# Kernel optimization log

Hardware: AMD Instinct MI355X
Metric: run time of the kernel (lower is better)

## Reference

```python
import jax, jax.numpy as jnp
import numpy as np

NEG = -1e9


def setup_inputs() -> dict:
    key = jax.random.key(0)
    ks = jax.random.split(key, 10)
    B, C, H, W = 4, 64, 64, 64
    Cq = C // 8
    x = jax.random.normal(ks[0], (B, C, H, W), dtype=jnp.float32)
    mask = jax.random.randint(ks[1], (B, 1, H, W), 0, 2, dtype=jnp.int32)
    # 1x1 conv params (out_ch, in_ch) + bias
    Wq = jax.random.normal(ks[2], (Cq, C), dtype=jnp.float32) * (1.0 / np.sqrt(C))
    bq = jnp.zeros((Cq,), dtype=jnp.float32)
    Wk = jax.random.normal(ks[3], (Cq, C), dtype=jnp.float32) * (1.0 / np.sqrt(C))
    bk = jnp.zeros((Cq,), dtype=jnp.float32)
    Wv = jax.random.normal(ks[4], (C, C), dtype=jnp.float32) * (1.0 / np.sqrt(C))
    bv = jnp.zeros((C,), dtype=jnp.float32)
    # torch inits gamma to 0; use small random so attention path contributes
    gamma = jax.random.normal(ks[5], (1,), dtype=jnp.float32) * 0.1
    return {"x": x, "mask": mask, "Wq": Wq, "bq": bq, "Wk": Wk, "bk": bk,
            "Wv": Wv, "bv": bv, "gamma": gamma}


def reference(x, mask, Wq, bq, Wk, bk, Wv, bv, gamma):
    B, C, H, W = x.shape
    N = H * W
    xf = x.reshape(B, C, N)                      # (B,C,N)
    # 1x1 convs == per-pixel linear projections
    q = jnp.einsum('oc,bcn->bno', Wq, xf) + bq   # (B,N,Cq)
    k = jnp.einsum('oc,bcn->bon', Wk, xf) + bk[None, :, None]  # (B,Cq,N)
    v = jnp.einsum('oc,bcn->bon', Wv, xf) + bv[None, :, None]  # (B,C,N)
    m = mask.reshape(B, N).astype(bool)
    logits = jnp.einsum('bno,bom->bnm', q, k)    # (B,N,N)
    valid = m[:, :, None] & m[:, None, :]        # outer-product validity mask
    logits = jnp.where(valid, logits, NEG)
    attn = jax.nn.softmax(logits, axis=-1)       # (B,N,N)
    out = jnp.einsum('bcj,bij->bci', v, attn)    # (B,C,N)
    out = out.reshape(B, C, H, W)
    return gamma * out + x
```

## Files before the change

### kernel.cpp

```cpp
#include <hip/hip_runtime.h>

typedef unsigned int uint;
typedef unsigned short ushort;
typedef __attribute__((ext_vector_type(8))) short short8;
typedef __attribute__((ext_vector_type(4))) float f32x4;
typedef __attribute__((ext_vector_type(16))) float f32x16;
typedef __attribute__((ext_vector_type(4))) uint uint4v;

#define BATCH 4
#define CH 64
#define NPIX 4096
#define LOG2E 1.44269504f

#define WSQ 0
#define WSK (BATCH * 128 * 512)
#define WSV (2 * BATCH * 128 * 512)

__device__ __forceinline__ ushort f2bf(float f) {
    union { float f; uint u; } a; a.f = f;
    const uint u = a.u;
    return (ushort)((u + 0x7FFFu + ((u >> 16) & 1u)) >> 16);
}
__device__ __forceinline__ uint pkbf(float a, float b) {
    return (uint)f2bf(a) | ((uint)f2bf(b) << 16);
}
__device__ __forceinline__ uint pkbf_fu(float a, float b) {
    union { float f; uint u; } x, y; x.f = a; y.f = b;
    return ((y.u + 0x8000u) & 0xFFFF0000u) | ((x.u + 0x8000u) >> 16);
}

__global__ __launch_bounds__(256) void proj_kernel(
    const float* __restrict__ x, const int* __restrict__ mask,
    const float* __restrict__ Wq, const float* __restrict__ bq,
    const float* __restrict__ Wk, const float* __restrict__ bk,
    const float* __restrict__ Wv, const float* __restrict__ bv,
    ushort* __restrict__ ws)
{
    __shared__ float wsh[16 * 64];
    __shared__ float bsh[16];
    const int g = blockIdx.y;
    const int tid = threadIdx.x;
    const int nout = (g == 0) ? 16 : 8;

    if (g == 0) {
        for (int i = tid; i < 512; i += 256) { wsh[i] = Wq[i]; wsh[512 + i] = Wk[i]; }
        if (tid < 8)  bsh[tid] = bq[tid];
        else if (tid < 16) bsh[tid] = bk[tid - 8];
    } else {
        const float* W = Wv + (g - 1) * 512;
        for (int i = tid; i < 512; i += 256) wsh[i] = W[i];
        if (tid < 8) bsh[tid] = bv[(g - 1) * 8 + tid];
    }
    __syncthreads();

    const int pix = blockIdx.x * 256 + tid;
    const int b = pix >> 12;
    const int n = pix & (NPIX - 1);
    const float* xb = x + (size_t)b * CH * NPIX + n;

    float acc[16];
#pragma unroll
    for (int o = 0; o < 16; o++) acc[o] = (o < nout) ? bsh[o] : 0.f;

#pragma unroll
    for (int c4 = 0; c4 < 16; c4++) {
        float xv0 = xb[(size_t)(c4 * 4 + 0) * NPIX];
        float xv1 = xb[(size_t)(c4 * 4 + 1) * NPIX];
        float xv2 = xb[(size_t)(c4 * 4 + 2) * NPIX];
        float xv3 = xb[(size_t)(c4 * 4 + 3) * NPIX];
        if (g == 0) {
#pragma unroll
            for (int o = 0; o < 16; o++) {
                const int base = (o < 8 ? 0 : 512) + (o & 7) * 64;
                float4 w = *(const float4*)&wsh[base + c4 * 4];
                acc[o] += w.x * xv0 + w.y * xv1 + w.z * xv2 + w.w * xv3;
            }
        } else {
#pragma unroll
            for (int o = 0; o < 8; o++) {
                float4 w = *(const float4*)&wsh[o * 64 + c4 * 4];
                acc[o] += w.x * xv0 + w.y * xv1 + w.z * xv2 + w.w * xv3;
            }
        }
    }

    const int jt = n >> 5, jl = n & 31;
    if (g == 0) {
        const int qm = mask[pix];
        {
            const float s = qm ? LOG2E : 0.f;
            uint4v lo, hi;
            lo.x = pkbf(acc[0] * s, acc[1] * s);
            lo.y = pkbf(acc[2] * s, acc[3] * s);
            lo.z = pkbf(acc[4] * s, acc[5] * s);
            lo.w = pkbf(acc[6] * s, acc[7] * s);
            hi.x = qm ? 0x3F80u : 0u;
            hi.y = 0u; hi.z = 0u; hi.w = 0u;
            ushort* qf = ws + WSQ + (size_t)b * 65536 + (size_t)jt * 512;
            *(uint4v*)(qf + jl * 8)       = lo;
            *(uint4v*)(qf + 256 + jl * 8) = hi;
        }
        {
            uint4v lo, hi;
            lo.x = pkbf(acc[8],  acc[9]);
            lo.y = pkbf(acc[10], acc[11]);
            lo.z = pkbf(acc[12], acc[13]);
            lo.w = pkbf(acc[14], acc[15]);
            hi.x = (uint)f2bf(qm ? 0.f : -1e30f);
            hi.y = 0u; hi.z = 0u; hi.w = 0u;
            ushort* kf = ws + WSK + (size_t)b * 65536 + (size_t)jt * 512;
            *(uint4v*)(kf + jl * 8)       = lo;
            *(uint4v*)(kf + 256 + jl * 8) = hi;
        }
    } else {
        const int h = jl >> 4, hp = (jl >> 3) & 1, jj = jl & 7;
        const int c0 = (g - 1) * 8;
        ushort* vt = ws + WSV + (size_t)b * 262144;
#pragma unroll
        for (int o = 0; o < 8; o++) {
            const int c = c0 + o, ct = c >> 5, cp = c & 31;
            vt[(size_t)((((jt * 2 + ct) * 2 + h) * 2 + hp) * 256) + cp * 8 + jj] = f2bf(acc[o]);
        }
    }
}

__global__ __launch_bounds__(256, 2) void attn_kernel(
    const ushort* __restrict__ ws, const float* __restrict__ x,
    const float* __restrict__ gamma, float* __restrict__ out)
{
    __shared__ float Obuf[4][64][36];
    __shared__ float Lbuf[4][32];
    __shared__ float Linv[32];

    const int tid  = threadIdx.x;
    const int wid  = tid >> 6;
    const int lane = tid & 63;
    const int hl   = lane >> 5;
    const int col  = lane & 31;
    const int b    = blockIdx.y;
    const int qt   = blockIdx.x;

    const ushort* qf = ws + WSQ + (size_t)b * 65536 + (size_t)qt * 512;
    const ushort* kf = ws + WSK + (size_t)b * 65536;
    const ushort* vt = ws + WSV + (size_t)b * 262144;

    const short8 qfrag = *(const short8*)(qf + lane * 8);

    f32x16 acc0, acc1, zf;
#pragma unroll
    for (int r = 0; r < 16; r++) { acc0[r] = 0.f; acc1[r] = 0.f; zf[r] = 0.f; }
    float lsum = 0.f;

    int jt = wid;
    uint4v kn   = *(const uint4v*)(kf + (size_t)jt * 512 + lane * 8);
    uint4v vn00 = *(const uint4v*)(vt + (size_t)((jt * 2 + 0) * 2 + 0) * 512 + lane * 8);
    uint4v vn01 = *(const uint4v*)(vt + (size_t)((jt * 2 + 0) * 2 + 1) * 512 + lane * 8);
    uint4v vn10 = *(const uint4v*)(vt + (size_t)((jt * 2 + 1) * 2 + 0) * 512 + lane * 8);
    uint4v vn11 = *(const uint4v*)(vt + (size_t)((jt * 2 + 1) * 2 + 1) * 512 + lane * 8);

    for (int t = 0; t < 32; t++) {
        const uint4v kc = kn, c00 = vn00, c01 = vn01, c10 = vn10, c11 = vn11;
        if (t < 31) {
            const int jn = jt + 4;
            kn   = *(const uint4v*)(kf + (size_t)jn * 512 + lane * 8);
            vn00 = *(const uint4v*)(vt + (size_t)((jn * 2 + 0) * 2 + 0) * 512 + lane * 8);
            vn01 = *(const uint4v*)(vt + (size_t)((jn * 2 + 0) * 2 + 1) * 512 + lane * 8);
            vn10 = *(const uint4v*)(vt + (size_t)((jn * 2 + 1) * 2 + 0) * 512 + lane * 8);
            vn11 = *(const uint4v*)(vt + (size_t)((jn * 2 + 1) * 2 + 1) * 512 + lane * 8);
        }

        const f32x16 s = __builtin_amdgcn_mfma_f32_32x32x16_bf16(
            *(const short8*)&kc, qfrag, zf, 0, 0, 0);

        float p[16];
#pragma unroll
        for (int r = 0; r < 16; r++) p[r] = __builtin_amdgcn_exp2f(s[r]);
#pragma unroll
        for (int r = 0; r < 16; r++) lsum += p[r];

        uint P[8];
#pragma unroll
        for (int r = 0; r < 8; r++) P[r] = pkbf_fu(p[2 * r], p[2 * r + 1]);
        uint S[8];
#pragma unroll
        for (int r = 0; r < 8; r++) S[r] = (uint)__shfl_xor((int)P[r], 32);

        uint4v B0v, B1v;
        B0v.x = hl ? S[2] : P[0];  B0v.y = hl ? S[3] : P[1];
        B0v.z = hl ? P[2] : S[0];  B0v.w = hl ? P[3] : S[1];
        B1v.x = hl ? S[6] : P[4];  B1v.y = hl ? S[7] : P[5];
        B1v.z = hl ? P[6] : S[4];  B1v.w = hl ? P[7] : S[5];

        acc0 = __builtin_amdgcn_mfma_f32_32x32x16_bf16(*(const short8*)&c00, *(const short8*)&B0v, acc0, 0, 0, 0);
        acc0 = __builtin_amdgcn_mfma_f32_32x32x16_bf16(*(const short8*)&c01, *(const short8*)&B1v, acc0, 0, 0, 0);
        acc1 = __builtin_amdgcn_mfma_f32_32x32x16_bf16(*(const short8*)&c10, *(const short8*)&B0v, acc1, 0, 0, 0);
        acc1 = __builtin_amdgcn_mfma_f32_32x32x16_bf16(*(const short8*)&c11, *(const short8*)&B1v, acc1, 0, 0, 0);

        jt += 4;
    }

    const float lw = lsum + __shfl_xor(lsum, 32);
#pragma unroll
    for (int r = 0; r < 16; r++) {
        const int crow = (r & 3) + 8 * (r >> 2) + 4 * hl;
        Obuf[wid][crow][col]      = acc0[r];
        Obuf[wid][32 + crow][col] = acc1[r];
    }
    if (hl == 0) Lbuf[wid][col] = lw;
    __syncthreads();
    if (tid < 32) Linv[tid] = 1.f / (Lbuf[0][tid] + Lbuf[1][tid] + Lbuf[2][tid] + Lbuf[3][tid]);
    __syncthreads();

    const float gm = gamma[0];
    const int c = tid >> 2, ms = (tid & 3) * 8;
    f32x4 o0 = {0.f, 0.f, 0.f, 0.f}, o1 = {0.f, 0.f, 0.f, 0.f};
#pragma unroll
    for (int w = 0; w < 4; w++) {
        o0 += *(const f32x4*)&Obuf[w][c][ms];
        o1 += *(const f32x4*)&Obuf[w][c][ms + 4];
    }
    const size_t base = (((size_t)(b * CH + c)) << 12) + qt * 32 + ms;
    const f32x4 x0 = *(const f32x4*)&x[base];
    const f32x4 x1 = *(const f32x4*)&x[base + 4];
    f32x4 r0, r1;
#pragma unroll
    for (int u = 0; u < 4; u++) {
        r0[u] = gm * o0[u] * Linv[ms + u]     + x0[u];
        r1[u] = gm * o1[u] * Linv[ms + 4 + u] + x1[u];
    }
    *(f32x4*)&out[base]     = r0;
    *(f32x4*)&out[base + 4] = r1;
}

extern "C" void kernel_launch(void* const* d_in, const int* in_sizes, int n_in,
                              void* d_out, int out_size, void* d_ws, size_t ws_size,
                              hipStream_t stream) {
    const float* x     = (const float*)d_in[0];
    const int*   mask  = (const int*)d_in[1];
    const float* Wq    = (const float*)d_in[2];
    const float* bq    = (const float*)d_in[3];
    const float* Wk    = (const float*)d_in[4];
    const float* bk    = (const float*)d_in[5];
    const float* Wv    = (const float*)d_in[6];
    const float* bv    = (const float*)d_in[7];
    const float* gamma = (const float*)d_in[8];
    float* out  = (float*)d_out;
    ushort* ws  = (ushort*)d_ws;

    proj_kernel<<<dim3(64, 9), 256, 0, stream>>>(x, mask, Wq, bq, Wk, bk, Wv, bv, ws);
    attn_kernel<<<dim3(128, 4), 256, 0, stream>>>(ws, x, gamma, out);
}
```

Measured before the change: 101.8 us.

## Process two query tiles per block with eight waves sharing K/V loads

Each block now handles two 32-query tiles with 512 threads (eight waves splitting the key range), so every K/V fragment loaded is reused for two QK and PV MFMA groups. This halves K/V global traffic per query. The lane shuffle is replaced with permlane32_swap, MFMAs are bracketed with s_setprio, and the row sum uses tree addition. The epilogue merges eight partial accumulators through shared memory in four passes, which adds extra barriers, more register pressure, and only 256 blocks.

Result: no change. 100.2 us (-1.6%).

```diff
diff --git a/kernel.cpp b/kernel.cpp
--- a/kernel.cpp
+++ b/kernel.cpp
@@ -6,6 +6,7 @@
 typedef __attribute__((ext_vector_type(4))) float f32x4;
 typedef __attribute__((ext_vector_type(16))) float f32x16;
 typedef __attribute__((ext_vector_type(4))) uint uint4v;
+typedef __attribute__((ext_vector_type(2))) uint uint2v;
 
 #define BATCH 4
 #define CH 64
@@ -124,13 +125,13 @@
     }
 }
 
-__global__ __launch_bounds__(256, 2) void attn_kernel(
+__global__ __launch_bounds__(512, 2) void attn_kernel(
     const ushort* __restrict__ ws, const float* __restrict__ x,
     const float* __restrict__ gamma, float* __restrict__ out)
 {
-    __shared__ float Obuf[4][64][36];
-    __shared__ float Lbuf[4][32];
-    __shared__ float Linv[32];
+    __shared__ float Obuf[8][32][36];
+    __shared__ float Lb[2][8][32];
+    __shared__ float Linv[2][32];
 
     const int tid  = threadIdx.x;
     const int wid  = tid >> 6;
@@ -138,18 +139,19 @@
     const int hl   = lane >> 5;
     const int col  = lane & 31;
     const int b    = blockIdx.y;
-    const int qt   = blockIdx.x;
-
-    const ushort* qf = ws + WSQ + (size_t)b * 65536 + (size_t)qt * 512;
+    const int bx   = blockIdx.x;
+
+    const ushort* qf = ws + WSQ + (size_t)b * 65536 + (size_t)(2 * bx) * 512;
     const ushort* kf = ws + WSK + (size_t)b * 65536;
     const ushort* vt = ws + WSV + (size_t)b * 262144;
 
-    const short8 qfrag = *(const short8*)(qf + lane * 8);
-
-    f32x16 acc0, acc1, zf;
-#pragma unroll
-    for (int r = 0; r < 16; r++) { acc0[r] = 0.f; acc1[r] = 0.f; zf[r] = 0.f; }
-    float lsum = 0.f;
+    const short8 qfA = *(const short8*)(qf + lane * 8);
+    const short8 qfB = *(const short8*)(qf + 512 + lane * 8);
+
+    f32x16 accA0, accA1, accB0, accB1, zf;
+#pragma unroll
+    for (int r = 0; r < 16; r++) { accA0[r] = 0.f; accA1[r] = 0.f; accB0[r] = 0.f; accB1[r] = 0.f; zf[r] = 0.f; }
+    float lsA = 0.f, lsB = 0.f;
 
     int jt = wid;
     uint4v kn   = *(const uint4v*)(kf + (size_t)jt * 512 + lane * 8);
@@ -158,10 +160,32 @@
     uint4v vn10 = *(const uint4v*)(vt + (size_t)((jt * 2 + 1) * 2 + 0) * 512 + lane * 8);
     uint4v vn11 = *(const uint4v*)(vt + (size_t)((jt * 2 + 1) * 2 + 1) * 512 + lane * 8);
 
-    for (int t = 0; t < 32; t++) {
+#define QK_PV(SFRAG, LSUM, A0, A1) do {                                                              \
+    float p[16];                                                                                     \
+    _Pragma("unroll") for (int r = 0; r < 16; r++) p[r] = __builtin_amdgcn_exp2f((SFRAG)[r]);        \
+    LSUM += (((p[0] + p[1]) + (p[2] + p[3])) + ((p[4] + p[5]) + (p[6] + p[7])))                      \
+          + (((p[8] + p[9]) + (p[10] + p[11])) + ((p[12] + p[13]) + (p[14] + p[15])));               \
+    uint P[8];                                                                                       \
+    _Pragma("unroll") for (int r = 0; r < 8; r++) P[r] = pkbf_fu(p[2 * r], p[2 * r + 1]);            \
+    const uint2v s02 = __builtin_amdgcn_permlane32_swap(P[0], P[2], false, false);                   \
+    const uint2v s13 = __builtin_amdgcn_permlane32_swap(P[1], P[3], false, false);                   \
+    const uint2v s46 = __builtin_amdgcn_permlane32_swap(P[4], P[6], false, false);                   \
+    const uint2v s57 = __builtin_amdgcn_permlane32_swap(P[5], P[7], false, false);                   \
+    uint4v B0, B1;                                                                                   \
+    B0.x = s02.x; B0.y = s13.x; B0.z = s02.y; B0.w = s13.y;                                          \
+    B1.x = s46.x; B1.y = s57.x; B1.z = s46.y; B1.w = s57.y;                                          \
+    __builtin_amdgcn_s_setprio(1);                                                                   \
+    A0 = __builtin_amdgcn_mfma_f32_32x32x16_bf16(*(const short8*)&c00, *(const short8*)&B0, A0, 0, 0, 0); \
+    A0 = __builtin_amdgcn_mfma_f32_32x32x16_bf16(*(const short8*)&c01, *(const short8*)&B1, A0, 0, 0, 0); \
+    A1 = __builtin_amdgcn_mfma_f32_32x32x16_bf16(*(const short8*)&c10, *(const short8*)&B0, A1, 0, 0, 0); \
+    A1 = __builtin_amdgcn_mfma_f32_32x32x16_bf16(*(const short8*)&c11, *(const short8*)&B1, A1, 0, 0, 0); \
+    __builtin_amdgcn_s_setprio(0);                                                                   \
+} while (0)
+
+    for (int t = 0; t < 16; t++) {
         const uint4v kc = kn, c00 = vn00, c01 = vn01, c10 = vn10, c11 = vn11;
-        if (t < 31) {
-            const int jn = jt + 4;
+        if (t < 15) {
+            const int jn = jt + 8;
             kn   = *(const uint4v*)(kf + (size_t)jn * 512 + lane * 8);
             vn00 = *(const uint4v*)(vt + (size_t)((jn * 2 + 0) * 2 + 0) * 512 + lane * 8);
             vn01 = *(const uint4v*)(vt + (size_t)((jn * 2 + 0) * 2 + 1) * 512 + lane * 8);
@@ -169,67 +193,55 @@
             vn11 = *(const uint4v*)(vt + (size_t)((jn * 2 + 1) * 2 + 1) * 512 + lane * 8);
         }
 
-        const f32x16 s = __builtin_amdgcn_mfma_f32_32x32x16_bf16(
-            *(const short8*)&kc, qfrag, zf, 0, 0, 0);
-
-        float p[16];
-#pragma unroll
-        for (int r = 0; r < 16; r++) p[r] = __builtin_amdgcn_exp2f(s[r]);
-#pragma unroll
-        for (int r = 0; r < 16; r++) lsum += p[r];
-
-        uint P[8];
-#pragma unroll
-        for (int r = 0; r < 8; r++) P[r] = pkbf_fu(p[2 * r], p[2 * r + 1]);
-        uint S[8];
-#pragma unroll
-        for (int r = 0; r < 8; r++) S[r] = (uint)__shfl_xor((int)P[r], 32);
-
-        uint4v B0v, B1v;
-        B0v.x = hl ? S[2] : P[0];  B0v.y = hl ? S[3] : P[1];
-        B0v.z = hl ? P[2] : S[0];  B0v.w = hl ? P[3] : S[1];
-        B1v.x = hl ? S[6] : P[4];  B1v.y = hl ? S[7] : P[5];
-        B1v.z = hl ? P[6] : S[4];  B1v.w = hl ? P[7] : S[5];
-
-        acc0 = __builtin_amdgcn_mfma_f32_32x32x16_bf16(*(const short8*)&c00, *(const short8*)&B0v, acc0, 0, 0, 0);
-        acc0 = __builtin_amdgcn_mfma_f32_32x32x16_bf16(*(const short8*)&c01, *(const short8*)&B1v, acc0, 0, 0, 0);
-        acc1 = __builtin_amdgcn_mfma_f32_32x32x16_bf16(*(const short8*)&c10, *(const short8*)&B0v, acc1, 0, 0, 0);
-        acc1 = __builtin_amdgcn_mfma_f32_32x32x16_bf16(*(const short8*)&c11, *(const short8*)&B1v, acc1, 0, 0, 0);
-
-        jt += 4;
-    }
-
-    const float lw = lsum + __shfl_xor(lsum, 32);
-#pragma unroll
-    for (int r = 0; r < 16; r++) {
-        const int crow = (r & 3) + 8 * (r >> 2) + 4 * hl;
-        Obuf[wid][crow][col]      = acc0[r];
-        Obuf[wid][32 + crow][col] = acc1[r];
-    }
-    if (hl == 0) Lbuf[wid][col] = lw;
+        const f32x16 sA = __builtin_amdgcn_mfma_f32_32x32x16_bf16(*(const short8*)&kc, qfA, zf, 0, 0, 0);
+        const f32x16 sB = __builtin_amdgcn_mfma_f32_32x32x16_bf16(*(const short8*)&kc, qfB, zf, 0, 0, 0);
+
+        QK_PV(sA, lsA, accA0, accA1);
+        QK_PV(sB, lsB, accB0, accB1);
+
+        jt += 8;
+    }
+#undef QK_PV
+
+    const float lwA = lsA + __shfl_xor(lsA, 32);
+    const float lwB = lsB + __shfl_xor(lsB, 32);
+    if (hl == 0) { Lb[0][wid][col] = lwA; Lb[1][wid][col] = lwB; }
     __syncthreads();
-    if (tid < 32) Linv[tid] = 1.f / (Lbuf[0][tid] + Lbuf[1][tid] + Lbuf[2][tid] + Lbuf[3][tid]);
-    __syncthreads();
+    if (tid < 64) {
+        const int q = tid >> 5, m = tid & 31;
+        float s = 0.f;
+#pragma unroll
+        for (int w = 0; w < 8; w++) s += Lb[q][w][m];
+        Linv[q][m] = 1.f / s;
+    }
 
     const float gm = gamma[0];
-    const int c = tid >> 2, ms = (tid & 3) * 8;
-    f32x4 o0 = {0.f, 0.f, 0.f, 0.f}, o1 = {0.f, 0.f, 0.f, 0.f};
-#pragma unroll
-    for (int w = 0; w < 4; w++) {
-        o0 += *(const f32x4*)&Obuf[w][c][ms];
-        o1 += *(const f32x4*)&Obuf[w][c][ms + 4];
-    }
-    const size_t base = (((size_t)(b * CH + c)) << 12) + qt * 32 + ms;
-    const f32x4 x0 = *(const f32x4*)&x[base];
-    const f32x4 x1 = *(const f32x4*)&x[base + 4];
-    f32x4 r0, r1;
-#pragma unroll
-    for (int u = 0; u < 4; u++) {
-        r0[u] = gm * o0[u] * Linv[ms + u]     + x0[u];
-        r1[u] = gm * o1[u] * Linv[ms + 4 + u] + x1[u];
-    }
-    *(f32x4*)&out[base]     = r0;
-    *(f32x4*)&out[base + 4] = r1;
+
+#define MERGE_PASS(ACC, QSEL, CHALF) do {                                                            \
+    __syncthreads();                                                                                 \
+    _Pragma("unroll") for (int r = 0; r < 16; r++) {                                                 \
+        const int crow = (r & 3) + 8 * (r >> 2) + 4 * hl;            \
+        Obuf[wid][crow][col] = (ACC)[r];                                                             \
+    }                                                                                                \
+    __syncthreads();                                                                                 \
+    {                                                                                                \
+        const int c = tid >> 4, m0 = (tid & 15) * 2;                                                 \
+        float o0 = 0.f, o1 = 0.f;                                                                    \
+        _Pragma("unroll") for (int w = 0; w < 8; w++) { o0 += Obuf[w][c][m0]; o1 += Obuf[w][c][m0 + 1]; } \
+        const size_t base = (((size_t)(b * CH + (CHALF) * 32 + c)) << 12) + bx * 64 + (QSEL) * 32 + m0; \
+        const float2 xv = *(const float2*)&x[base];                                                  \
+        float2 rv;                                                                                   \
+        rv.x = gm * o0 * Linv[QSEL][m0]     + xv.x;                                                  \
+        rv.y = gm * o1 * Linv[QSEL][m0 + 1] + xv.y;                                                  \
+        *(float2*)&out[base] = rv;                                                                   \
+    }                                                                                                \
+} while (0)
+
+    MERGE_PASS(accA0, 0, 0);
+    MERGE_PASS(accA1, 0, 1);
+    MERGE_PASS(accB0, 1, 0);
+    MERGE_PASS(accB1, 1, 1);
+#undef MERGE_PASS
 }
 
 extern "C" void kernel_launch(void* const* d_in, const int* in_sizes, int n_in,
@@ -248,5 +260,5 @@
     ushort* ws  = (ushort*)d_ws;
 
     proj_kernel<<<dim3(64, 9), 256, 0, stream>>>(x, mask, Wq, bq, Wk, bk, Wv, bv, ws);
-    attn_kernel<<<dim3(128, 4), 256, 0, stream>>>(ws, x, gamma, out);
-}
+    attn_kernel<<<dim3(64, 4), 512, 0, stream>>>(ws, x, gamma, out);
+}
```
